# Optimization experiments

Hardware: AMD Instinct MI355X
Metric: run time of the kernel (lower is better)

The kernel has to match this reference:

```python
import jax, jax.numpy as jnp
import numpy as np

N, IN, C, H, NC, E, G = 4096, 16, 128, 2, 4, 131072, 64
EPS = 1e-5


def setup_inputs() -> dict:
    key = jax.random.key(0)
    ks = jax.random.split(key, 12)
    def rn(k, shape, scale=0.05):
        return jax.random.normal(k, shape, dtype=jnp.float32) * scale
    return dict(
        x=rn(ks[0], (N, IN), 1.0),
        edge_index=jax.random.randint(ks[1], (2, E), 0, N, dtype=jnp.int32),
        batch=jnp.sort(jax.random.randint(ks[2], (N,), 0, G, dtype=jnp.int32)),
        proj_W=rn(ks[3], (IN, C)), proj_b=jnp.zeros((C,), jnp.float32),
        gcn_W=rn(ks[4], (2, C, C)), gcn_b=jnp.zeros((2, C), jnp.float32),
        attn_qkv_w=rn(ks[5], (2, 3 * C, C)), attn_qkv_b=jnp.zeros((2, 3 * C), jnp.float32),
        attn_out_w=rn(ks[6], (2, C, C)), attn_out_b=jnp.zeros((2, C), jnp.float32),
        bn_gamma=jnp.ones((2, 3, C), jnp.float32), bn_beta=jnp.zeros((2, 3, C), jnp.float32),
        mlp_W1=rn(ks[7], (2, C, 2 * C)), mlp_b1=jnp.zeros((2, 2 * C), jnp.float32),
        mlp_W2=rn(ks[8], (2, 2 * C, C)), mlp_b2=jnp.zeros((2, C), jnp.float32),
        lin_W=rn(ks[9], (C, NC)), lin_b=jnp.zeros((NC,), jnp.float32),
    )


def _bn(h, g, b):
    # PyG BatchNorm (training-mode stats over the node dim, biased var)
    mu = jnp.mean(h, axis=0)
    var = jnp.mean((h - mu) ** 2, axis=0)
    return (h - mu) * jax.lax.rsqrt(var + EPS) * g + b


def _gcn(h_in, W, b, src, dst):
    # GCNConv: x' = D^-1/2 (A+I) D^-1/2 (x W) + b
    h = h_in @ W
    deg = jnp.zeros((N,), h.dtype).at[dst].add(1.0) + 1.0  # +1 self loop
    dinv = jax.lax.rsqrt(deg)
    coef = dinv[src] * dinv[dst]                           # [E]
    out = jax.ops.segment_sum(h[src] * coef[:, None], dst, num_segments=N)
    out = out + h * (dinv * dinv)[:, None]                 # self-loop term
    return out + b


def _mha(x, wqkv, bqkv, wout, bout):
    # batch=None in the source => attention over all N nodes as one sequence
    qkv = x @ wqkv.T + bqkv                                # [N,3C]
    q, k, v = jnp.split(qkv, 3, axis=-1)
    dh = C // H
    q = q.reshape(N, H, dh) * (dh ** -0.5)
    k = k.reshape(N, H, dh)
    v = v.reshape(N, H, dh)
    a = jax.nn.softmax(jnp.einsum('nhd,mhd->hnm', q, k), axis=-1)  # [H,N,N]
    o = jnp.einsum('hnm,mhd->nhd', a, v).reshape(N, C)
    return o @ wout.T + bout


def _forward(x, proj_W, proj_b, gcn_W, gcn_b, attn_qkv_w, attn_qkv_b,
             attn_out_w, attn_out_b, bn_gamma, bn_beta, mlp_W1, mlp_b1,
             mlp_W2, mlp_b2, lin_W, lin_b, edge_index, batch):
    src, dst = edge_index[0], edge_index[1]
    h = x @ proj_W + proj_b
    for l in range(2):  # two structurally-distinct GPS layers
        hl = _bn(_gcn(h, gcn_W[l], gcn_b[l], src, dst) + h, bn_gamma[l, 0], bn_beta[l, 0])
        ha = _bn(_mha(h, attn_qkv_w[l], attn_qkv_b[l], attn_out_w[l], attn_out_b[l]) + h,
                 bn_gamma[l, 1], bn_beta[l, 1])
        o = hl + ha
        m = jax.nn.relu(o @ mlp_W1[l] + mlp_b1[l]) @ mlp_W2[l] + mlp_b2[l]
        h = _bn(o + m, bn_gamma[l, 2], bn_beta[l, 2])
        if l == 0:
            h = jax.nn.relu(h)
    ssum = jax.ops.segment_sum(h, batch, num_segments=G)
    cnt = jax.ops.segment_sum(jnp.ones((N,), h.dtype), batch, num_segments=G)
    pooled = ssum / jnp.maximum(cnt, 1.0)[:, None]
    return pooled @ lin_W + lin_b


def reference(x, edge_index, batch, proj_W, proj_b, gcn_W, gcn_b,
              attn_qkv_w, attn_qkv_b, attn_out_w, attn_out_b,
              bn_gamma, bn_beta, mlp_W1, mlp_b1, mlp_W2, mlp_b2,
              lin_W, lin_b):
    return _forward(x, proj_W, proj_b, gcn_W, gcn_b, attn_qkv_w, attn_qkv_b,
                    attn_out_w, attn_out_b, bn_gamma, bn_beta, mlp_W1, mlp_b1,
                    mlp_W2, mlp_b2, lin_W, lin_b, edge_index, batch)
```

## Files before the change

### kernel.cpp

```cpp
#include <hip/hip_runtime.h>
#include <hip/hip_bf16.h>


constexpr int N_  = 4096;
constexpr int IN_ = 16;
constexpr int C_  = 128;
constexpr int E_  = 131072;
constexpr int G_  = 64;
constexpr float EPSV = 1e-5f;
constexpr int SP_ = 8;

typedef unsigned short u16;
typedef unsigned int u32;
typedef __attribute__((ext_vector_type(8))) short bf16x8;
typedef __attribute__((ext_vector_type(4))) short bf16x4;
typedef __attribute__((ext_vector_type(8))) unsigned short u16x8;
typedef __attribute__((ext_vector_type(4))) float f32x4;

__device__ inline u16 f2bf(float f) {
  union { __hip_bfloat16 b; u16 u; } v;
  v.b = __float2bfloat16(f);
  return v.u;
}
__device__ inline float bf2f(u16 s) {
  union { unsigned u; float f; } v; v.u = ((unsigned)s) << 16;
  return v.f;
}

__global__ __launch_bounds__(256) void prol_k(const float* __restrict__ x,
                                              const float* __restrict__ projW,
                                              const float* __restrict__ projB,
                                              float* __restrict__ h,
                                              const float* __restrict__ gcnW,
                                              const float* __restrict__ qkvW,
                                              const float* __restrict__ outW,
                                              const float* __restrict__ w1,
                                              const float* __restrict__ w2,
                                              u16* __restrict__ Wh,
                                              u16* __restrict__ Wl,
                                              const int* __restrict__ ei,
                                              int* __restrict__ cnt) {
  const int bx = blockIdx.x;
  const int tid = threadIdx.x;
  if (bx < 2048) {
    int idx = bx * 256 + tid;
    int n = idx >> 7, c = idx & 127;
    float acc = projB[c];
#pragma unroll
    for (int k = 0; k < IN_; ++k) acc = fmaf(x[n * IN_ + k], projW[k * C_ + c], acc);
    h[idx] = acc;
    return;
  }
  if (bx >= 2336) {
    int e = (bx - 2336) * 256 + tid;
    atomicAdd(&cnt[ei[E_ + e]], 1);
    return;
  }
  int wb = bx - 2048;
  int l = wb / 144, b = wb % 144;
  const float* src; int dstOff, K, M, trans;
  if (b < 16)       { src = gcnW + l * 16384; dstOff = 0;      K = 128; M = 128; trans = 0; }
  else if (b < 64)  { src = qkvW + l * 49152; dstOff = 16384;  K = 128; M = 0;   trans = 1; b -= 16; }
  else if (b < 80)  { src = outW + l * 16384; dstOff = 65536;  K = 128; M = 0;   trans = 1; b -= 64; }
  else if (b < 112) { src = w1 + l * 32768;   dstOff = 81920;  K = 128; M = 256; trans = 0; b -= 80; }
  else              { src = w2 + l * 32768;   dstOff = 114688; K = 256; M = 128; trans = 0; b -= 112; }
  dstOff += l * 147456;
  int d = b * 1024 + tid * 4;
  float v[4];
  if (trans) {
    const float4 f = *(const float4*)&src[d];
    v[0] = f.x; v[1] = f.y; v[2] = f.z; v[3] = f.w;
  } else {
    int ks = (K == 256) ? 8 : 7;
    int n = d >> ks, k = d & (K - 1);
#pragma unroll
    for (int j = 0; j < 4; ++j) v[j] = src[(size_t)(k + j) * M + n];
  }
  ushort4 hv, lv;
  u16* hp = (u16*)&hv; u16* lp = (u16*)&lv;
#pragma unroll
  for (int j = 0; j < 4; ++j) {
    u16 hh = f2bf(v[j]); hp[j] = hh; lp[j] = f2bf(v[j] - bf2f(hh));
  }
  *(ushort4*)&Wh[dstOff + d] = hv;
  *(ushort4*)&Wl[dstOff + d] = lv;
}

__global__ __launch_bounds__(256) void scan_k(const int* __restrict__ cnt,
                                              int* __restrict__ rowptr,
                                              int* __restrict__ cursor,
                                              float* __restrict__ dinv) {
  __shared__ int part[256];
  const int t = threadIdx.x;
  int v[16], s = 0;
#pragma unroll
  for (int i = 0; i < 16; ++i) { v[i] = cnt[t * 16 + i]; s += v[i]; }
  part[t] = s;
  __syncthreads();
  if (t == 0) {
    int run = 0;
    for (int i = 0; i < 256; ++i) { int x = part[i]; part[i] = run; run += x; }
  }
  __syncthreads();
  int off = part[t];
#pragma unroll
  for (int i = 0; i < 16; ++i) {
    int n = t * 16 + i;
    rowptr[n] = off; cursor[n] = off;
    dinv[n] = rsqrtf((float)v[i] + 1.0f);
    off += v[i];
  }
  if (t == 0) rowptr[N_] = E_;
}

__global__ __launch_bounds__(256) void mgemm_dual_k(const float* __restrict__ A,
                                                    const u16* __restrict__ Bh,
                                                    const u16* __restrict__ Bl,
                                                    const float* __restrict__ qkvB,
                                                    float* __restrict__ t0,
                                                    u16* __restrict__ Qg,
                                                    u16* __restrict__ Kg,
                                                    u16* __restrict__ Vtg,
                                                    const int* __restrict__ ei,
                                                    int* __restrict__ cursor,
                                                    int* __restrict__ csr) {
  constexpr int LD = 72, K = 128;
  __shared__ u16 Ah[64 * LD], Al[64 * LD], Bsh[64 * LD], Bsl[64 * LD];
  const int bx = blockIdx.x;
  const int tid = threadIdx.x;
  if (bx >= 512) {
    int e = (bx - 512) * 256 + tid;
    int d = ei[E_ + e];
    int slot = atomicAdd(&cursor[d], 1);
    csr[slot] = ei[e];
    return;
  }
  const int row0 = (bx >> 3) * 64, col0 = (bx & 7) * 64;
  const int wv = tid >> 6, ln = tid & 63, quad = ln >> 4, c = ln & 15;
  f32x4 acc[4];
#pragma unroll
  for (int i = 0; i < 4; ++i) acc[i] = (f32x4){0.f, 0.f, 0.f, 0.f};

  for (int kt = 0; kt < K; kt += 64) {
    __syncthreads();
#pragma unroll
    for (int i = 0; i < 2; ++i) {
      int ch = tid + i * 256, r = ch >> 3, part = ch & 7;
      const float4 f0 = *(const float4*)&A[(size_t)(row0 + r) * K + kt + part * 8];
      const float4 f1 = *(const float4*)&A[(size_t)(row0 + r) * K + kt + part * 8 + 4];
      float fv[8] = {f0.x, f0.y, f0.z, f0.w, f1.x, f1.y, f1.z, f1.w};
      __attribute__((aligned(16))) u16 hb[8], lb[8];
#pragma unroll
      for (int j = 0; j < 8; ++j) {
        u16 hh = f2bf(fv[j]); hb[j] = hh; lb[j] = f2bf(fv[j] - bf2f(hh));
      }
      *(u16x8*)&Ah[r * LD + part * 8] = *(u16x8*)hb;
      *(u16x8*)&Al[r * LD + part * 8] = *(u16x8*)lb;
      size_t bo = (size_t)(col0 + r) * K + kt + part * 8;
      *(u16x8*)&Bsh[r * LD + part * 8] = *(const u16x8*)&Bh[bo];
      *(u16x8*)&Bsl[r * LD + part * 8] = *(const u16x8*)&Bl[bo];
    }
    __syncthreads();
#pragma unroll
    for (int kq = 0; kq < 2; ++kq) {
      bf16x8 ah = *(const bf16x8*)&Ah[(wv * 16 + c) * LD + kq * 32 + quad * 8];
      bf16x8 al = *(const bf16x8*)&Al[(wv * 16 + c) * LD + kq * 32 + quad * 8];
#pragma unroll
      for (int cb = 0; cb < 4; ++cb) {
        bf16x8 bh = *(const bf16x8*)&Bsh[(cb * 16 + c) * LD + kq * 32 + quad * 8];
        bf16x8 bl = *(const bf16x8*)&Bsl[(cb * 16 + c) * LD + kq * 32 + quad * 8];
        acc[cb] = __builtin_amdgcn_mfma_f32_16x16x32_bf16(al, bh, acc[cb], 0, 0, 0);
        acc[cb] = __builtin_amdgcn_mfma_f32_16x16x32_bf16(ah, bl, acc[cb], 0, 0, 0);
        acc[cb] = __builtin_amdgcn_mfma_f32_16x16x32_bf16(ah, bh, acc[cb], 0, 0, 0);
      }
    }
  }

  const int cls = bx & 7;
  if (cls < 2) {
#pragma unroll
    for (int cb = 0; cb < 4; ++cb)
#pragma unroll
      for (int r = 0; r < 4; ++r) {
        int rr = row0 + wv * 16 + quad * 4 + r;
        t0[(size_t)rr * 128 + col0 + cb * 16 + c] = acc[cb][r];
      }
  } else if (cls < 6) {
    const int isQ = cls < 4, hd = cls & 1;
    const float sc = isQ ? 0.125f : 1.0f;
    u16* dst = isQ ? Qg : Kg;
#pragma unroll
    for (int cb = 0; cb < 4; ++cb) {
      int d = cb * 16 + c;
      float qb = qkvB[col0 - 128 + d];
#pragma unroll
      for (int r = 0; r < 4; ++r) {
        int rr = row0 + wv * 16 + quad * 4 + r;
        dst[((size_t)(hd * N_ + rr)) * 64 + d] = f2bf((acc[cb][r] + qb) * sc);
      }
    }
  } else {
    const int hd = cls & 1;
    u16* vtile = Ah;
    __syncthreads();
#pragma unroll
    for (int cb = 0; cb < 4; ++cb) {
      int d = cb * 16 + c;
      float vb = qkvB[col0 - 128 + d];
#pragma unroll
      for (int r = 0; r < 4; ++r)
        vtile[(wv * 16 + quad * 4 + r) * LD + d] = f2bf(acc[cb][r] + vb);
    }
    __syncthreads();
    int d = tid >> 2, j = tid & 3;
    __attribute__((aligned(16))) u16 buf[16];
#pragma unroll
    for (int m = 0; m < 16; ++m) buf[m] = vtile[(j * 16 + m) * LD + d];
    size_t o = ((size_t)(hd * 64 + d)) * N_ + row0 + j * 16;
    *(u16x8*)&Vtg[o]     = *(u16x8*)&buf[0];
    *(u16x8*)&Vtg[o + 8] = *(u16x8*)&buf[8];
  }
}

__global__ __launch_bounds__(256) void mgemm_k(const float* __restrict__ A,
                                               const u16* __restrict__ Bh,
                                               const u16* __restrict__ Bl,
                                               const float* __restrict__ bias,
                                               float* __restrict__ Cout,
                                               int K, int Ncols, int relu,
                                               const float* __restrict__ resid,
                                               float* __restrict__ sums) {
  constexpr int LD = 72;
  __shared__ u16 Ah[64 * LD], Al[64 * LD], Bsh[64 * LD], Bsl[64 * LD];
  const int tid = threadIdx.x;
  const int row0 = blockIdx.y * 64, col0 = blockIdx.x * 64;
  const int wv = tid >> 6, ln = tid & 63, quad = ln >> 4, c = ln & 15;
  f32x4 acc[4];
#pragma unroll
  for (int i = 0; i < 4; ++i) acc[i] = (f32x4){0.f, 0.f, 0.f, 0.f};

  for (int kt = 0; kt < K; kt += 64) {
    __syncthreads();
#pragma unroll
    for (int i = 0; i < 2; ++i) {
      int ch = tid + i * 256, r = ch >> 3, part = ch & 7;
      const float4 f0 = *(const float4*)&A[(size_t)(row0 + r) * K + kt + part * 8];
      const float4 f1 = *(const float4*)&A[(size_t)(row0 + r) * K + kt + part * 8 + 4];
      float fv[8] = {f0.x, f0.y, f0.z, f0.w, f1.x, f1.y, f1.z, f1.w};
      __attribute__((aligned(16))) u16 hb[8], lb[8];
#pragma unroll
      for (int j = 0; j < 8; ++j) {
        u16 hh = f2bf(fv[j]); hb[j] = hh; lb[j] = f2bf(fv[j] - bf2f(hh));
      }
      *(u16x8*)&Ah[r * LD + part * 8] = *(u16x8*)hb;
      *(u16x8*)&Al[r * LD + part * 8] = *(u16x8*)lb;
      size_t bo = (size_t)(col0 + r) * K + kt + part * 8;
      *(u16x8*)&Bsh[r * LD + part * 8] = *(const u16x8*)&Bh[bo];
      *(u16x8*)&Bsl[r * LD + part * 8] = *(const u16x8*)&Bl[bo];
    }
    __syncthreads();
#pragma unroll
    for (int kq = 0; kq < 2; ++kq) {
      bf16x8 ah = *(const bf16x8*)&Ah[(wv * 16 + c) * LD + kq * 32 + quad * 8];
      bf16x8 al = *(const bf16x8*)&Al[(wv * 16 + c) * LD + kq * 32 + quad * 8];
#pragma unroll
      for (int cb = 0; cb < 4; ++cb) {
        bf16x8 bh = *(const bf16x8*)&Bsh[(cb * 16 + c) * LD + kq * 32 + quad * 8];
        bf16x8 bl = *(const bf16x8*)&Bsl[(cb * 16 + c) * LD + kq * 32 + quad * 8];
        acc[cb] = __builtin_amdgcn_mfma_f32_16x16x32_bf16(al, bh, acc[cb], 0, 0, 0);
        acc[cb] = __builtin_amdgcn_mfma_f32_16x16x32_bf16(ah, bl, acc[cb], 0, 0, 0);
        acc[cb] = __builtin_amdgcn_mfma_f32_16x16x32_bf16(ah, bh, acc[cb], 0, 0, 0);
      }
    }
  }
#pragma unroll
  for (int cb = 0; cb < 4; ++cb) {
    float s = 0.0f, s2 = 0.0f;
#pragma unroll
    for (int r = 0; r < 4; ++r) {
      int rr = row0 + wv * 16 + quad * 4 + r;
      int cc = col0 + cb * 16 + c;
      float o = acc[cb][r] + (bias ? bias[cc] : 0.0f);
      if (resid) o += resid[(size_t)rr * Ncols + cc];
      if (relu) o = fmaxf(o, 0.0f);
      Cout[(size_t)rr * Ncols + cc] = o;
      s += o; s2 = fmaf(o, o, s2);
    }
    if (sums) {
      s  += __shfl_xor(s, 16);  s  += __shfl_xor(s, 32);
      s2 += __shfl_xor(s2, 16); s2 += __shfl_xor(s2, 32);
      if (quad == 0) {
        int cc = col0 + cb * 16 + c;
        atomicAdd(&sums[cc], s);
        atomicAdd(&sums[C_ + cc], s2);
      }
    }
  }
}

__global__ __launch_bounds__(256) void mgemm_attn_k(const float* __restrict__ attnP,
                                                    const float* __restrict__ accLp,
                                                    const u16* __restrict__ Bh,
                                                    const u16* __restrict__ Bl,
                                                    const float* __restrict__ bias,
                                                    float* __restrict__ Cout,
                                                    const float* __restrict__ resid,
                                                    float* __restrict__ sums) {
  constexpr int LD = 72, K = 128;
  __shared__ u16 Ah[64 * LD], Al[64 * LD], Bsh[64 * LD], Bsl[64 * LD];
  const int tid = threadIdx.x;
  const int row0 = blockIdx.y * 64, col0 = blockIdx.x * 64;
  const int wv = tid >> 6, ln = tid & 63, quad = ln >> 4, c = ln & 15;
  f32x4 acc[4];
#pragma unroll
  for (int i = 0; i < 4; ++i) acc[i] = (f32x4){0.f, 0.f, 0.f, 0.f};

  for (int kt = 0; kt < K; kt += 64) {
    const int head = kt >> 6;
    __syncthreads();
#pragma unroll
    for (int i = 0; i < 2; ++i) {
      int ch = tid + i * 256, r = ch >> 3, part = ch & 7;
      float lsum = 0.0f;
#pragma unroll
      for (int sp = 0; sp < SP_; ++sp) lsum += accLp[(sp * 2 + head) * N_ + row0 + r];
      float invl = 1.0f / lsum;
      float fv[8] = {0.f, 0.f, 0.f, 0.f, 0.f, 0.f, 0.f, 0.f};
#pragma unroll
      for (int sp = 0; sp < SP_; ++sp) {
        const float* p = &attnP[((size_t)sp * N_ + row0 + r) * C_ + kt + part * 8];
        const float4 f0 = *(const float4*)p;
        const float4 f1 = *(const float4*)(p + 4);
        fv[0] += f0.x; fv[1] += f0.y; fv[2] += f0.z; fv[3] += f0.w;
        fv[4] += f1.x; fv[5] += f1.y; fv[6] += f1.z; fv[7] += f1.w;
      }
      __attribute__((aligned(16))) u16 hb[8], lb[8];
#pragma unroll
      for (int j = 0; j < 8; ++j) {
        float f = fv[j] * invl;
        u16 hh = f2bf(f); hb[j] = hh; lb[j] = f2bf(f - bf2f(hh));
      }
      *(u16x8*)&Ah[r * LD + part * 8] = *(u16x8*)hb;
      *(u16x8*)&Al[r * LD + part * 8] = *(u16x8*)lb;
      size_t bo = (size_t)(col0 + r) * K + kt + part * 8;
      *(u16x8*)&Bsh[r * LD + part * 8] = *(const u16x8*)&Bh[bo];
      *(u16x8*)&Bsl[r * LD + part * 8] = *(const u16x8*)&Bl[bo];
    }
    __syncthreads();
#pragma unroll
    for (int kq = 0; kq < 2; ++kq) {
      bf16x8 ah = *(const bf16x8*)&Ah[(wv * 16 + c) * LD + kq * 32 + quad * 8];
      bf16x8 al = *(const bf16x8*)&Al[(wv * 16 + c) * LD + kq * 32 + quad * 8];
#pragma unroll
      for (int cb = 0; cb < 4; ++cb) {
        bf16x8 bh = *(const bf16x8*)&Bsh[(cb * 16 + c) * LD + kq * 32 + quad * 8];
        bf16x8 bl = *(const bf16x8*)&Bsl[(cb * 16 + c) * LD + kq * 32 + quad * 8];
        acc[cb] = __builtin_amdgcn_mfma_f32_16x16x32_bf16(al, bh, acc[cb], 0, 0, 0);
        acc[cb] = __builtin_amdgcn_mfma_f32_16x16x32_bf16(ah, bl, acc[cb], 0, 0, 0);
        acc[cb] = __builtin_amdgcn_mfma_f32_16x16x32_bf16(ah, bh, acc[cb], 0, 0, 0);
      }
    }
  }
#pragma unroll
  for (int cb = 0; cb < 4; ++cb) {
    float s = 0.0f, s2 = 0.0f;
#pragma unroll
    for (int r = 0; r < 4; ++r) {
      int rr = row0 + wv * 16 + quad * 4 + r;
      int cc = col0 + cb * 16 + c;
      float o = acc[cb][r] + bias[cc] + resid[(size_t)rr * 128 + cc];
      Cout[(size_t)rr * 128 + cc] = o;
      s += o; s2 = fmaf(o, o, s2);
    }
    s  += __shfl_xor(s, 16);  s  += __shfl_xor(s, 32);
    s2 += __shfl_xor(s2, 16); s2 += __shfl_xor(s2, 32);
    if (quad == 0) {
      int cc = col0 + cb * 16 + c;
      atomicAdd(&sums[cc], s);
      atomicAdd(&sums[C_ + cc], s2);
    }
  }
}

__global__ __launch_bounds__(256) void branch_k(const u16* __restrict__ Qg,
                                                const u16* __restrict__ Kg,
                                                const u16* __restrict__ Vtg,
                                                float* __restrict__ attnP,
                                                float* __restrict__ accLp,
                                                const int* __restrict__ rowptr,
                                                const int* __restrict__ csr,
                                                const float* __restrict__ hw,
                                                const float* __restrict__ dinv,
                                                const float* __restrict__ gbias,
                                                const float* __restrict__ hres,
                                                float* __restrict__ t1,
                                                float* __restrict__ sums0) {
  constexpr int LD = 72;
  __shared__ __attribute__((aligned(16))) u16 smem[2 * 64 * LD];
  const int tid = threadIdx.x;
  const int bx = blockIdx.x;

  if (bx >= 512) {
    const int b = bx - 512;
    const int wq = tid >> 6, lane = tid & 63;
    const int n = b * 4 + wq;
    float* ls  = (float*)smem;
    float* ls2 = ls + 512;
    const float din = dinv[n];
    float a0 = fmaf(hw[(size_t)n * C_ + lane], din * din,
                    gbias[lane] + hres[(size_t)n * C_ + lane]);
    float a1 = fmaf(hw[(size_t)n * C_ + lane + 64], din * din,
                    gbias[lane + 64] + hres[(size_t)n * C_ + lane + 64]);
    const int e1 = rowptr[n + 1];
    int e = rowptr[n];
    for (; e + 4 <= e1; e += 4) {
      int s0 = csr[e], s1 = csr[e + 1], s2i = csr[e + 2], s3 = csr[e + 3];
      float w0 = dinv[s0] * din, w1 = dinv[s1] * din;
      float w2 = dinv[s2i] * din, w3 = dinv[s3] * din;
      float x00 = hw[(size_t)s0 * C_ + lane],  x01 = hw[(size_t)s0 * C_ + lane + 64];
      float x10 = hw[(size_t)s1 * C_ + lane],  x11 = hw[(size_t)s1 * C_ + lane + 64];
      float x20 = hw[(size_t)s2i * C_ + lane], x21 = hw[(size_t)s2i * C_ + lane + 64];
      float x30 = hw[(size_t)s3 * C_ + lane],  x31 = hw[(size_t)s3 * C_ + lane + 64];
      a0 = fmaf(x00, w0, a0); a1 = fmaf(x01, w0, a1);
      a0 = fmaf(x10, w1, a0); a1 = fmaf(x11, w1, a1);
      a0 = fmaf(x20, w2, a0); a1 = fmaf(x21, w2, a1);
      a0 = fmaf(x30, w3, a0); a1 = fmaf(x31, w3, a1);
    }
    for (; e < e1; ++e) {
      int si = csr[e];
      float w = dinv[si] * din;
      a0 = fmaf(hw[(size_t)si * C_ + lane], w, a0);
      a1 = fmaf(hw[(size_t)si * C_ + lane + 64], w, a1);
    }
    t1[(size_t)n * C_ + lane]      = a0;
    t1[(size_t)n * C_ + lane + 64] = a1;
    ls[wq * 128 + lane]       = a0;  ls[wq * 128 + lane + 64]  = a1;
    ls2[wq * 128 + lane]      = a0 * a0;
    ls2[wq * 128 + lane + 64] = a1 * a1;
    __syncthreads();
    if (tid < 128) {
      float s  = ls[tid]  + ls[tid + 128]  + ls[tid + 256]  + ls[tid + 384];
      float s2 = ls2[tid] + ls2[tid + 128] + ls2[tid + 256] + ls2[tid + 384];
      atomicAdd(&sums0[tid], s);
      atomicAdd(&sums0[C_ + tid], s2);
    }
    return;
  }

  u16* Ks  = smem;
  u16* Vts = smem + 64 * LD;
  const int fb = bx;
  const int head = fb >> 8, sp = (fb >> 5) & 7, q0 = (fb & 31) * 128;
  const int wv = tid >> 6, ln = tid & 63, quad = ln >> 4, c = ln & 15;
  const int KPS = N_ / SP_;
  const int qb = q0 + wv * 32;

  bf16x8 qfA[2], qfB[2];
#pragma unroll
  for (int kq = 0; kq < 2; ++kq) {
    qfA[kq] = *(const bf16x8*)&Qg[((size_t)(head * N_ + qb + c)) * 64 + kq * 32 + quad * 8];
    qfB[kq] = *(const bf16x8*)&Qg[((size_t)(head * N_ + qb + 16 + c)) * 64 + kq * 32 + quad * 8];
  }

  f32x4 OA[4], OB[4];
#pragma unroll
  for (int i = 0; i < 4; ++i) {
    OA[i] = (f32x4){0.f, 0.f, 0.f, 0.f};
    OB[i] = (f32x4){0.f, 0.f, 0.f, 0.f};
  }
  float lsumA = 0.0f, lsumB = 0.0f;

  for (int it = 0; it < KPS / 64; ++it) {
    const int k0 = sp * KPS + it * 64;
    __syncthreads();
#pragma unroll
    for (int i = 0; i < 2; ++i) {
      int ch = tid + i * 256, row = ch >> 3, part = ch & 7;
      *(u16x8*)&Ks[row * LD + part * 8] =
          *(const u16x8*)&Kg[((size_t)(head * N_ + k0 + row)) * 64 + part * 8];
      *(u16x8*)&Vts[row * LD + part * 8] =
          *(const u16x8*)&Vtg[((size_t)(head * 64 + row)) * N_ + k0 + part * 8];
    }
    __syncthreads();

    bf16x4 pfA[4], pfB[4];
#pragma unroll
    for (int kb = 0; kb < 4; ++kb) {
      f32x4 stA = (f32x4){0.f, 0.f, 0.f, 0.f};
      f32x4 stB = (f32x4){0.f, 0.f, 0.f, 0.f};
#pragma unroll
      for (int kq = 0; kq < 2; ++kq) {
        bf16x8 a = *(const bf16x8*)&Ks[(kb * 16 + c) * LD + kq * 32 + quad * 8];
        stA = __builtin_amdgcn_mfma_f32_16x16x32_bf16(a, qfA[kq], stA, 0, 0, 0);
        stB = __builtin_amdgcn_mfma_f32_16x16x32_bf16(a, qfB[kq], stB, 0, 0, 0);
      }
      u16 a0 = f2bf(__expf(stA[0] - 8.0f));
      u16 a1 = f2bf(__expf(stA[1] - 8.0f));
      u16 a2 = f2bf(__expf(stA[2] - 8.0f));
      u16 a3 = f2bf(__expf(stA[3] - 8.0f));
      lsumA += bf2f(a0) + bf2f(a1) + bf2f(a2) + bf2f(a3);
      pfA[kb] = (bf16x4){(short)a0, (short)a1, (short)a2, (short)a3};
      u16 b0 = f2bf(__expf(stB[0] - 8.0f));
      u16 b1 = f2bf(__expf(stB[1] - 8.0f));
      u16 b2 = f2bf(__expf(stB[2] - 8.0f));
      u16 b3 = f2bf(__expf(stB[3] - 8.0f));
      lsumB += bf2f(b0) + bf2f(b1) + bf2f(b2) + bf2f(b3);
      pfB[kb] = (bf16x4){(short)b0, (short)b1, (short)b2, (short)b3};
    }

#pragma unroll
    for (int db = 0; db < 4; ++db) {
#pragma unroll
      for (int kb = 0; kb < 4; ++kb) {
        bf16x4 va = *(const bf16x4*)&Vts[(db * 16 + c) * LD + kb * 16 + quad * 4];
        OA[db] = __builtin_amdgcn_mfma_f32_16x16x16bf16_1k(va, pfA[kb], OA[db], 0, 0, 0);
        OB[db] = __builtin_amdgcn_mfma_f32_16x16x16bf16_1k(va, pfB[kb], OB[db], 0, 0, 0);
      }
    }
  }

  lsumA += __shfl_xor(lsumA, 16); lsumA += __shfl_xor(lsumA, 32);
  lsumB += __shfl_xor(lsumB, 16); lsumB += __shfl_xor(lsumB, 32);
  if (ln < 16) {
    accLp[(sp * 2 + head) * N_ + qb + c]      = lsumA;
    accLp[(sp * 2 + head) * N_ + qb + 16 + c] = lsumB;
  }

  constexpr int LDO = 68;
  float* OT = (float*)smem;
  __syncthreads();
#pragma unroll
  for (int hh = 0; hh < 2; ++hh) {
    if ((wv >> 1) == hh) {
      const int lq = (wv & 1) * 32;
#pragma unroll
      for (int db = 0; db < 4; ++db)
#pragma unroll
        for (int r = 0; r < 4; ++r) {
          OT[(lq + c) * LDO + db * 16 + quad * 4 + r]      = OA[db][r];
          OT[(lq + 16 + c) * LDO + db * 16 + quad * 4 + r] = OB[db][r];
        }
    }
    __syncthreads();
    {
      const int q_loc = tid >> 2, dblk = tid & 3;
      const float4* srcv = (const float4*)&OT[q_loc * LDO + dblk * 16];
      float4* dstv = (float4*)&attnP[((size_t)sp * N_ + q0 + hh * 64 + q_loc) * C_ + head * 64 + dblk * 16];
#pragma unroll
      for (int j = 0; j < 4; ++j) dstv[j] = srcv[j];
    }
    if (hh == 0) __syncthreads();
  }
}

__global__ __launch_bounds__(256) void bn_finapply2_k(const float* __restrict__ t0,
                                                      const float* __restrict__ t1,
                                                      const float* __restrict__ sums1,
                                                      const float* __restrict__ sums0,
                                                      const float* __restrict__ g1,
                                                      const float* __restrict__ b1v,
                                                      const float* __restrict__ g0,
                                                      const float* __restrict__ b0v,
                                                      float* __restrict__ ob) {
  __shared__ float scl1[128], shf1[128], scl0[128], shf0[128];
  const int t = threadIdx.x;
  if (t < 128) {
    float mu = sums1[t] * (1.0f / N_);
    float var = sums1[C_ + t] * (1.0f / N_) - mu * mu;
    float sc = rsqrtf(var + EPSV) * g1[t];
    scl1[t] = sc; shf1[t] = fmaf(-mu, sc, b1v[t]);
    mu = sums0[t] * (1.0f / N_);
    var = sums0[C_ + t] * (1.0f / N_) - mu * mu;
    sc = rsqrtf(var + EPSV) * g0[t];
    scl0[t] = sc; shf0[t] = fmaf(-mu, sc, b0v[t]);
  }
  __syncthreads();
  int idx = blockIdx.x * 256 + t;
  int c = idx & 127;
  ob[idx] = fmaf(t0[idx], scl1[c], shf1[c]) + fmaf(t1[idx], scl0[c], shf0[c]);
}

__global__ __launch_bounds__(256) void bn_finapply_k(const float* __restrict__ A,
                                                     const float* __restrict__ sums,
                                                     const float* __restrict__ g,
                                                     const float* __restrict__ b,
                                                     float* __restrict__ outp, int relu,
                                                     const int* __restrict__ batch,
                                                     float* __restrict__ pooled) {
  __shared__ float s_scl[128], s_shf[128];
  const int t = threadIdx.x;
  if (t < 128) {
    float mu = sums[t] * (1.0f / N_);
    float var = sums[C_ + t] * (1.0f / N_) - mu * mu;
    float sc = rsqrtf(var + EPSV) * g[t];
    s_scl[t] = sc;
    s_shf[t] = fmaf(-mu, sc, b[t]);
  }
  __syncthreads();
  int idx = blockIdx.x * 256 + t;
  int c = idx & 127;
  float v = fmaf(A[idx], s_scl[c], s_shf[c]);
  if (relu) v = fmaxf(v, 0.0f);
  outp[idx] = v;
  if (pooled) {
    int n = idx >> 7;
    atomicAdd(&pooled[(size_t)batch[n] * C_ + c], v);
  }
}

__global__ __launch_bounds__(256) void final_k(const float* __restrict__ pooled,
                                               const int* __restrict__ batch,
                                               const float* __restrict__ W,
                                               const float* __restrict__ b,
                                               float* __restrict__ out) {
  int t = threadIdx.x;
  int g = t >> 2, j = t & 3;
  int lo = 0, hi = N_;
  while (lo < hi) { int m = (lo + hi) >> 1; if (batch[m] < g) lo = m + 1; else hi = m; }
  int st = lo; lo = 0; hi = N_;
  while (lo < hi) { int m = (lo + hi) >> 1; if (batch[m] < g + 1) lo = m + 1; else hi = m; }
  float inv = 1.0f / fmaxf((float)(lo - st), 1.0f);
  float acc = b[j];
  for (int c = 0; c < C_; ++c) acc = fmaf(pooled[(size_t)g * C_ + c] * inv, W[c * 4 + j], acc);
  out[t] = acc;
}

extern "C" void kernel_launch(void* const* d_in, const int* in_sizes, int n_in,
                              void* d_out, int out_size, void* d_ws, size_t ws_size,
                              hipStream_t stream) {
  const float* x     = (const float*)d_in[0];
  const int*   ei    = (const int*)d_in[1];
  const int*   batch = (const int*)d_in[2];
  const float* projW = (const float*)d_in[3];
  const float* projB = (const float*)d_in[4];
  const float* gcnW  = (const float*)d_in[5];
  const float* gcnB  = (const float*)d_in[6];
  const float* qkvW  = (const float*)d_in[7];
  const float* qkvB  = (const float*)d_in[8];
  const float* outW  = (const float*)d_in[9];
  const float* outB  = (const float*)d_in[10];
  const float* bnG   = (const float*)d_in[11];
  const float* bnB   = (const float*)d_in[12];
  const float* w1    = (const float*)d_in[13];
  const float* b1    = (const float*)d_in[14];
  const float* w2    = (const float*)d_in[15];
  const float* b2    = (const float*)d_in[16];
  const float* linW  = (const float*)d_in[17];
  const float* linB  = (const float*)d_in[18];
  float* out = (float*)d_out;

  const size_t NC = (size_t)N_ * C_;
  const size_t HB = (size_t)2 * N_ * 64;
  float* ws   = (float*)d_ws;
  float* h    = ws;
  float* t0   = ws + 1 * NC;
  float* t1   = ws + 2 * NC;
  float* ob   = ws + 3 * NC;
  u16* Qg  = (u16*)(ws + 4 * NC);
  u16* Kg  = Qg + HB;
  u16* Vtg = Kg + HB;
  float* attnP = ws + 6 * NC;
  float* m1b   = attnP;
  float* accLp = ws + (6 + SP_) * NC;
  float* sums  = accLp + 2 * SP_ * N_;
  float* pooled = sums + 6 * 256;
  int*   icnt = (int*)(pooled + (size_t)G_ * C_);
  float* dinv = (float*)(icnt + N_);
  int*   rowptr = (int*)(dinv + N_);
  int*   cursor = rowptr + N_ + 1;
  int*   csr    = cursor + N_;
  u16*   Wh = (u16*)(csr + E_);
  u16*   Wl = Wh + 2 * 147456;

  const dim3 b256(256);

  hipMemsetAsync(sums, 0, (6 * 256 + (size_t)G_ * C_ + N_) * sizeof(float), stream);

  prol_k<<<2848, b256, 0, stream>>>(x, projW, projB, h, gcnW, qkvW, outW,
                                    w1, w2, Wh, Wl, ei, icnt);
  scan_k<<<1, b256, 0, stream>>>(icnt, rowptr, cursor, dinv);

  for (int l = 0; l < 2; ++l) {
    const size_t WL = (size_t)l * 147456;
    float* sums0 = sums + (l * 3 + 0) * 256;
    float* sums1 = sums + (l * 3 + 1) * 256;
    float* sums2 = sums + (l * 3 + 2) * 256;

    mgemm_dual_k<<<(l == 0) ? 1024 : 512, b256, 0, stream>>>(
        h, Wh + WL, Wl + WL, qkvB + l * 384, t0, Qg, Kg, Vtg, ei, cursor, csr);
    branch_k<<<1536, b256, 0, stream>>>(Qg, Kg, Vtg, attnP, accLp,
                                        rowptr, csr, t0, dinv, gcnB + l * C_,
                                        h, t1, sums0);
    mgemm_attn_k<<<dim3(2, 64), b256, 0, stream>>>(attnP, accLp,
                                                   Wh + WL + 65536, Wl + WL + 65536,
                                                   outB + l * C_, t0, h, sums1);
    bn_finapply2_k<<<(int)(NC / 256), b256, 0, stream>>>(
        t0, t1, sums1, sums0,
        bnG + (l * 3 + 1) * C_, bnB + (l * 3 + 1) * C_,
        bnG + (l * 3 + 0) * C_, bnB + (l * 3 + 0) * C_, ob);
    mgemm_k<<<dim3(4, 64), b256, 0, stream>>>(ob, Wh + WL + 81920, Wl + WL + 81920,
                                              b1 + l * 256, m1b, 128, 256, 1,
                                              nullptr, nullptr);
    mgemm_k<<<dim3(2, 64), b256, 0, stream>>>(m1b, Wh + WL + 114688, Wl + WL + 114688,
                                              b2 + l * C_, t0, 256, 128, 0,
                                              ob, sums2);
    bn_finapply_k<<<(int)(NC / 256), b256, 0, stream>>>(
        t0, sums2, bnG + (l * 3 + 2) * C_, bnB + (l * 3 + 2) * C_, h,
        (l == 0) ? 1 : 0, batch, (l == 1) ? pooled : nullptr);
  }

  final_k<<<1, 256, 0, stream>>>(pooled, batch, linW, linB, out);
}
```

Before: 316.2 us.

## Fuse BN applies into following GEMMs, double-buffer attention K/V, vectorize projection

Removes the standalone bn_finapply2 kernel by folding the two BN applies and their sum into the MLP1 GEMM's A-tile load, and folds the layer-0 final BN+ReLU into the layer-1 dual GEMM's A load (one column block writes h back). The attention loop now prefetches the next K/V tile into registers and double-buffers shared memory, which cuts one barrier per iteration. The input projection in the prologue is vectorized to four outputs per thread, so it needs fewer blocks. These changes trade extra per-block BN recomputation and doubled LDS use in branch_k for fewer launches and less global round-tripping.

```diff
diff --git a/kernel.cpp b/kernel.cpp
--- a/kernel.cpp
+++ b/kernel.cpp
@@ -42,21 +42,31 @@
                                               int* __restrict__ cnt) {
   const int bx = blockIdx.x;
   const int tid = threadIdx.x;
-  if (bx < 2048) {
-    int idx = bx * 256 + tid;
-    int n = idx >> 7, c = idx & 127;
-    float acc = projB[c];
-#pragma unroll
-    for (int k = 0; k < IN_; ++k) acc = fmaf(x[n * IN_ + k], projW[k * C_ + c], acc);
-    h[idx] = acc;
+  if (bx < 512) {
+    int base = (bx * 256 + tid) * 4;
+    int n = base >> 7, c = base & 127;
+    const float4* xr = (const float4*)&x[n * IN_];
+    float4 x0 = xr[0], x1 = xr[1], x2 = xr[2], x3 = xr[3];
+    float xv[16] = {x0.x, x0.y, x0.z, x0.w, x1.x, x1.y, x1.z, x1.w,
+                    x2.x, x2.y, x2.z, x2.w, x3.x, x3.y, x3.z, x3.w};
+    float4 acc = *(const float4*)&projB[c];
+#pragma unroll
+    for (int k = 0; k < IN_; ++k) {
+      float4 wv = *(const float4*)&projW[k * C_ + c];
+      acc.x = fmaf(xv[k], wv.x, acc.x);
+      acc.y = fmaf(xv[k], wv.y, acc.y);
+      acc.z = fmaf(xv[k], wv.z, acc.z);
+      acc.w = fmaf(xv[k], wv.w, acc.w);
+    }
+    *(float4*)&h[base] = acc;
     return;
   }
-  if (bx >= 2336) {
-    int e = (bx - 2336) * 256 + tid;
+  if (bx >= 800) {
+    int e = (bx - 800) * 256 + tid;
     atomicAdd(&cnt[ei[E_ + e]], 1);
     return;
   }
-  int wb = bx - 2048;
+  int wb = bx - 512;
   int l = wb / 144, b = wb % 144;
   const float* src; int dstOff, K, M, trans;
   if (b < 16)       { src = gcnW + l * 16384; dstOff = 0;      K = 128; M = 128; trans = 0; }
@@ -117,15 +127,20 @@
                                                     const u16* __restrict__ Bh,
                                                     const u16* __restrict__ Bl,
                                                     const float* __restrict__ qkvB,
-                                                    float* __restrict__ t0,
+                                                    float* __restrict__ hwOut,
                                                     u16* __restrict__ Qg,
                                                     u16* __restrict__ Kg,
                                                     u16* __restrict__ Vtg,
                                                     const int* __restrict__ ei,
                                                     int* __restrict__ cursor,
-                                                    int* __restrict__ csr) {
+                                                    int* __restrict__ csr,
+                                                    const float* __restrict__ bnsums,
+                                                    const float* __restrict__ bng,
+                                                    const float* __restrict__ bnb,
+                                                    float* __restrict__ hOut) {
   constexpr int LD = 72, K = 128;
   __shared__ u16 Ah[64 * LD], Al[64 * LD], Bsh[64 * LD], Bsl[64 * LD];
+  __shared__ float s_scl[128], s_shf[128];
   const int bx = blockIdx.x;
   const int tid = threadIdx.x;
   if (bx >= 512) {
@@ -137,6 +152,12 @@
   }
   const int row0 = (bx >> 3) * 64, col0 = (bx & 7) * 64;
   const int wv = tid >> 6, ln = tid & 63, quad = ln >> 4, c = ln & 15;
+  if (bnsums && tid < 128) {
+    float mu = bnsums[tid] * (1.0f / N_);
+    float var = bnsums[C_ + tid] * (1.0f / N_) - mu * mu;
+    float sc = rsqrtf(var + EPSV) * bng[tid];
+    s_scl[tid] = sc; s_shf[tid] = fmaf(-mu, sc, bnb[tid]);
+  }
   f32x4 acc[4];
 #pragma unroll
   for (int i = 0; i < 4; ++i) acc[i] = (f32x4){0.f, 0.f, 0.f, 0.f};
@@ -146,9 +167,19 @@
 #pragma unroll
     for (int i = 0; i < 2; ++i) {
       int ch = tid + i * 256, r = ch >> 3, part = ch & 7;
-      const float4 f0 = *(const float4*)&A[(size_t)(row0 + r) * K + kt + part * 8];
-      const float4 f1 = *(const float4*)&A[(size_t)(row0 + r) * K + kt + part * 8 + 4];
+      const int kk = kt + part * 8;
+      const float4 f0 = *(const float4*)&A[(size_t)(row0 + r) * K + kk];
+      const float4 f1 = *(const float4*)&A[(size_t)(row0 + r) * K + kk + 4];
       float fv[8] = {f0.x, f0.y, f0.z, f0.w, f1.x, f1.y, f1.z, f1.w};
+      if (bnsums) {
+#pragma unroll
+        for (int j = 0; j < 8; ++j)
+          fv[j] = fmaxf(fmaf(fv[j], s_scl[kk + j], s_shf[kk + j]), 0.0f);
+        if ((bx & 7) == 0) {
+          *(float4*)&hOut[(size_t)(row0 + r) * K + kk]     = (float4){fv[0], fv[1], fv[2], fv[3]};
+          *(float4*)&hOut[(size_t)(row0 + r) * K + kk + 4] = (float4){fv[4], fv[5], fv[6], fv[7]};
+        }
+      }
       __attribute__((aligned(16))) u16 hb[8], lb[8];
 #pragma unroll
       for (int j = 0; j < 8; ++j) {
@@ -156,7 +187,7 @@
       }
       *(u16x8*)&Ah[r * LD + part * 8] = *(u16x8*)hb;
       *(u16x8*)&Al[r * LD + part * 8] = *(u16x8*)lb;
-      size_t bo = (size_t)(col0 + r) * K + kt + part * 8;
+      size_t bo = (size_t)(col0 + r) * K + kk;
       *(u16x8*)&Bsh[r * LD + part * 8] = *(const u16x8*)&Bh[bo];
       *(u16x8*)&Bsl[r * LD + part * 8] = *(const u16x8*)&Bl[bo];
     }
@@ -183,7 +214,7 @@
 #pragma unroll
       for (int r = 0; r < 4; ++r) {
         int rr = row0 + wv * 16 + quad * 4 + r;
-        t0[(size_t)rr * 128 + col0 + cb * 16 + c] = acc[cb][r];
+        hwOut[(size_t)rr * 128 + col0 + cb * 16 + c] = acc[cb][r];
       }
   } else if (cls < 6) {
     const int isQ = cls < 4, hd = cls & 1;
@@ -298,6 +329,98 @@
   }
 }
 
+__global__ __launch_bounds__(256) void mgemm_mlp1_k(const float* __restrict__ t0,
+                                                    const float* __restrict__ t1,
+                                                    const float* __restrict__ sums1,
+                                                    const float* __restrict__ sums0,
+                                                    const float* __restrict__ g1,
+                                                    const float* __restrict__ b1v,
+                                                    const float* __restrict__ g0,
+                                                    const float* __restrict__ b0v,
+                                                    const u16* __restrict__ Bh,
+                                                    const u16* __restrict__ Bl,
+                                                    const float* __restrict__ bias,
+                                                    float* __restrict__ Cout,
+                                                    float* __restrict__ obOut) {
+  constexpr int LD = 72, K = 128, Ncols = 256;
+  __shared__ u16 Ah[64 * LD], Al[64 * LD], Bsh[64 * LD], Bsl[64 * LD];
+  __shared__ float s_scl1[128], s_shf1[128], s_scl0[128], s_shf0[128];
+  const int tid = threadIdx.x;
+  const int row0 = blockIdx.y * 64, col0 = blockIdx.x * 64;
+  const int wv = tid >> 6, ln = tid & 63, quad = ln >> 4, c = ln & 15;
+  if (tid < 128) {
+    float mu = sums1[tid] * (1.0f / N_);
+    float var = sums1[C_ + tid] * (1.0f / N_) - mu * mu;
+    float sc = rsqrtf(var + EPSV) * g1[tid];
+    s_scl1[tid] = sc; s_shf1[tid] = fmaf(-mu, sc, b1v[tid]);
+    mu = sums0[tid] * (1.0f / N_);
+    var = sums0[C_ + tid] * (1.0f / N_) - mu * mu;
+    sc = rsqrtf(var + EPSV) * g0[tid];
+    s_scl0[tid] = sc; s_shf0[tid] = fmaf(-mu, sc, b0v[tid]);
+  }
+  f32x4 acc[4];
+#pragma unroll
+  for (int i = 0; i < 4; ++i) acc[i] = (f32x4){0.f, 0.f, 0.f, 0.f};
+
+  for (int kt = 0; kt < K; kt += 64) {
+    __syncthreads();
+#pragma unroll
+    for (int i = 0; i < 2; ++i) {
+      int ch = tid + i * 256, r = ch >> 3, part = ch & 7;
+      const int kk = kt + part * 8;
+      const float4 a0 = *(const float4*)&t0[(size_t)(row0 + r) * K + kk];
+      const float4 a1 = *(const float4*)&t0[(size_t)(row0 + r) * K + kk + 4];
+      const float4 c0 = *(const float4*)&t1[(size_t)(row0 + r) * K + kk];
+      const float4 c1 = *(const float4*)&t1[(size_t)(row0 + r) * K + kk + 4];
+      float av[8] = {a0.x, a0.y, a0.z, a0.w, a1.x, a1.y, a1.z, a1.w};
+      float cv[8] = {c0.x, c0.y, c0.z, c0.w, c1.x, c1.y, c1.z, c1.w};
+      float fv[8];
+#pragma unroll
+      for (int j = 0; j < 8; ++j)
+        fv[j] = fmaf(av[j], s_scl1[kk + j], s_shf1[kk + j]) +
+                fmaf(cv[j], s_scl0[kk + j], s_shf0[kk + j]);
+      if (blockIdx.x == 0) {
+        *(float4*)&obOut[(size_t)(row0 + r) * K + kk]     = (float4){fv[0], fv[1], fv[2], fv[3]};
+        *(float4*)&obOut[(size_t)(row0 + r) * K + kk + 4] = (float4){fv[4], fv[5], fv[6], fv[7]};
+      }
+      __attribute__((aligned(16))) u16 hb[8], lb[8];
+#pragma unroll
+      for (int j = 0; j < 8; ++j) {
+        u16 hh = f2bf(fv[j]); hb[j] = hh; lb[j] = f2bf(fv[j] - bf2f(hh));
+      }
+      *(u16x8*)&Ah[r * LD + part * 8] = *(u16x8*)hb;
+      *(u16x8*)&Al[r * LD + part * 8] = *(u16x8*)lb;
+      size_t bo = (size_t)(col0 + r) * K + kk;
+      *(u16x8*)&Bsh[r * LD + part * 8] = *(const u16x8*)&Bh[bo];
+      *(u16x8*)&Bsl[r * LD + part * 8] = *(const u16x8*)&Bl[bo];
+    }
+    __syncthreads();
+#pragma unroll
+    for (int kq = 0; kq < 2; ++kq) {
+      bf16x8 ah = *(const bf16x8*)&Ah[(wv * 16 + c) * LD + kq * 32 + quad * 8];
+      bf16x8 al = *(const bf16x8*)&Al[(wv * 16 + c) * LD + kq * 32 + quad * 8];
+#pragma unroll
+      for (int cb = 0; cb < 4; ++cb) {
+        bf16x8 bh = *(const bf16x8*)&Bsh[(cb * 16 + c) * LD + kq * 32 + quad * 8];
+        bf16x8 bl = *(const bf16x8*)&Bsl[(cb * 16 + c) * LD + kq * 32 + quad * 8];
+        acc[cb] = __builtin_amdgcn_mfma_f32_16x16x32_bf16(al, bh, acc[cb], 0, 0, 0);
+        acc[cb] = __builtin_amdgcn_mfma_f32_16x16x32_bf16(ah, bl, acc[cb], 0, 0, 0);
+        acc[cb] = __builtin_amdgcn_mfma_f32_16x16x32_bf16(ah, bh, acc[cb], 0, 0, 0);
+      }
+    }
+  }
+#pragma unroll
+  for (int cb = 0; cb < 4; ++cb) {
+#pragma unroll
+    for (int r = 0; r < 4; ++r) {
+      int rr = row0 + wv * 16 + quad * 4 + r;
+      int cc = col0 + cb * 16 + c;
+      float o = fmaxf(acc[cb][r] + bias[cc], 0.0f);
+      Cout[(size_t)rr * Ncols + cc] = o;
+    }
+  }
+}
+
 __global__ __launch_bounds__(256) void mgemm_attn_k(const float* __restrict__ attnP,
                                                     const float* __restrict__ accLp,
                                                     const u16* __restrict__ Bh,
@@ -396,7 +519,7 @@
                                                 float* __restrict__ t1,
                                                 float* __restrict__ sums0) {
   constexpr int LD = 72;
-  __shared__ __attribute__((aligned(16))) u16 smem[2 * 64 * LD];
+  __shared__ __attribute__((aligned(16))) u16 smem[4 * 64 * LD];
   const int tid = threadIdx.x;
   const int bx = blockIdx.x;
 
@@ -447,12 +570,11 @@
     return;
   }
 
-  u16* Ks  = smem;
-  u16* Vts = smem + 64 * LD;
   const int fb = bx;
   const int head = fb >> 8, sp = (fb >> 5) & 7, q0 = (fb & 31) * 128;
   const int wv = tid >> 6, ln = tid & 63, quad = ln >> 4, c = ln & 15;
   const int KPS = N_ / SP_;
+  const int NIT = KPS / 64;
   const int qb = q0 + wv * 32;
 
   bf16x8 qfA[2], qfB[2];
@@ -470,18 +592,33 @@
   }
   float lsumA = 0.0f, lsumB = 0.0f;
 
-  for (int it = 0; it < KPS / 64; ++it) {
-    const int k0 = sp * KPS + it * 64;
-    __syncthreads();
-#pragma unroll
-    for (int i = 0; i < 2; ++i) {
-      int ch = tid + i * 256, row = ch >> 3, part = ch & 7;
-      *(u16x8*)&Ks[row * LD + part * 8] =
-          *(const u16x8*)&Kg[((size_t)(head * N_ + k0 + row)) * 64 + part * 8];
-      *(u16x8*)&Vts[row * LD + part * 8] =
-          *(const u16x8*)&Vtg[((size_t)(head * 64 + row)) * N_ + k0 + part * 8];
-    }
-    __syncthreads();
+  const int r0s = tid >> 3, p0s = tid & 7;
+  const int r1s = r0s + 32;
+  u16x8 kr0, kr1, vr0, vr1;
+  {
+    const int k0 = sp * KPS;
+    kr0 = *(const u16x8*)&Kg[((size_t)(head * N_ + k0 + r0s)) * 64 + p0s * 8];
+    kr1 = *(const u16x8*)&Kg[((size_t)(head * N_ + k0 + r1s)) * 64 + p0s * 8];
+    vr0 = *(const u16x8*)&Vtg[((size_t)(head * 64 + r0s)) * N_ + k0 + p0s * 8];
+    vr1 = *(const u16x8*)&Vtg[((size_t)(head * 64 + r1s)) * N_ + k0 + p0s * 8];
+    u16* K0 = smem;
+    *(u16x8*)&K0[r0s * LD + p0s * 8]            = kr0;
+    *(u16x8*)&K0[r1s * LD + p0s * 8]            = kr1;
+    *(u16x8*)&K0[64 * LD + r0s * LD + p0s * 8]  = vr0;
+    *(u16x8*)&K0[64 * LD + r1s * LD + p0s * 8]  = vr1;
+  }
+  __syncthreads();
+
+  for (int it = 0; it < NIT; ++it) {
+    u16* Ks  = smem + (it & 1) * 2 * 64 * LD;
+    u16* Vts = Ks + 64 * LD;
+    if (it + 1 < NIT) {
+      const int kn = sp * KPS + (it + 1) * 64;
+      kr0 = *(const u16x8*)&Kg[((size_t)(head * N_ + kn + r0s)) * 64 + p0s * 8];
+      kr1 = *(const u16x8*)&Kg[((size_t)(head * N_ + kn + r1s)) * 64 + p0s * 8];
+      vr0 = *(const u16x8*)&Vtg[((size_t)(head * 64 + r0s)) * N_ + kn + p0s * 8];
+      vr1 = *(const u16x8*)&Vtg[((size_t)(head * 64 + r1s)) * N_ + kn + p0s * 8];
+    }
 
     bf16x4 pfA[4], pfB[4];
 #pragma unroll
@@ -517,6 +654,15 @@
         OB[db] = __builtin_amdgcn_mfma_f32_16x16x16bf16_1k(va, pfB[kb], OB[db], 0, 0, 0);
       }
     }
+
+    if (it + 1 < NIT) {
+      u16* Kn = smem + ((it + 1) & 1) * 2 * 64 * LD;
+      *(u16x8*)&Kn[r0s * LD + p0s * 8]           = kr0;
+      *(u16x8*)&Kn[r1s * LD + p0s * 8]           = kr1;
+      *(u16x8*)&Kn[64 * LD + r0s * LD + p0s * 8] = vr0;
+      *(u16x8*)&Kn[64 * LD + r1s * LD + p0s * 8] = vr1;
+    }
+    __syncthreads();
   }
 
   lsumA += __shfl_xor(lsumA, 16); lsumA += __shfl_xor(lsumA, 32);
@@ -528,7 +674,6 @@
 
   constexpr int LDO = 68;
   float* OT = (float*)smem;
-  __syncthreads();
 #pragma unroll
   for (int hh = 0; hh < 2; ++hh) {
     if ((wv >> 1) == hh) {
@@ -551,33 +696,6 @@
     }
     if (hh == 0) __syncthreads();
   }
-}
-
-__global__ __launch_bounds__(256) void bn_finapply2_k(const float* __restrict__ t0,
-                                                      const float* __restrict__ t1,
-                                                      const float* __restrict__ sums1,
-                                                      const float* __restrict__ sums0,
-                                                      const float* __restrict__ g1,
-                                                      const float* __restrict__ b1v,
-                                                      const float* __restrict__ g0,
-                                                      const float* __restrict__ b0v,
-                                                      float* __restrict__ ob) {
-  __shared__ float scl1[128], shf1[128], scl0[128], shf0[128];
-  const int t = threadIdx.x;
-  if (t < 128) {
-    float mu = sums1[t] * (1.0f / N_);
-    float var = sums1[C_ + t] * (1.0f / N_) - mu * mu;
-    float sc = rsqrtf(var + EPSV) * g1[t];
-    scl1[t] = sc; shf1[t] = fmaf(-mu, sc, b1v[t]);
-    mu = sums0[t] * (1.0f / N_);
-    var = sums0[C_ + t] * (1.0f / N_) - mu * mu;
-    sc = rsqrtf(var + EPSV) * g0[t];
-    scl0[t] = sc; shf0[t] = fmaf(-mu, sc, b0v[t]);
-  }
-  __syncthreads();
-  int idx = blockIdx.x * 256 + t;
-  int c = idx & 127;
-  ob[idx] = fmaf(t0[idx], scl1[c], shf1[c]) + fmaf(t1[idx], scl0[c], shf0[c]);
 }
 
 __global__ __launch_bounds__(256) void bn_finapply_k(const float* __restrict__ A,
@@ -601,7 +719,7 @@
   int c = idx & 127;
   float v = fmaf(A[idx], s_scl[c], s_shf[c]);
   if (relu) v = fmaxf(v, 0.0f);
-  outp[idx] = v;
+  if (outp) outp[idx] = v;
   if (pooled) {
     int n = idx >> 7;
     atomicAdd(&pooled[(size_t)batch[n] * C_ + c], v);
@@ -676,7 +794,7 @@
 
   hipMemsetAsync(sums, 0, (6 * 256 + (size_t)G_ * C_ + N_) * sizeof(float), stream);
 
-  prol_k<<<2848, b256, 0, stream>>>(x, projW, projB, h, gcnW, qkvW, outW,
+  prol_k<<<1312, b256, 0, stream>>>(x, projW, projB, h, gcnW, qkvW, outW,
                                     w1, w2, Wh, Wl, ei, icnt);
   scan_k<<<1, b256, 0, stream>>>(icnt, rowptr, cursor, dinv);
 
@@ -685,28 +803,31 @@
     float* sums0 = sums + (l * 3 + 0) * 256;
     float* sums1 = sums + (l * 3 + 1) * 256;
     float* sums2 = sums + (l * 3 + 2) * 256;
+    const float* hwsrc = (l == 0) ? t0 : ob;
 
     mgemm_dual_k<<<(l == 0) ? 1024 : 512, b256, 0, stream>>>(
-        h, Wh + WL, Wl + WL, qkvB + l * 384, t0, Qg, Kg, Vtg, ei, cursor, csr);
+        (l == 0) ? h : t0, Wh + WL, Wl + WL, qkvB + l * 384,
+        (float*)hwsrc, Qg, Kg, Vtg, ei, cursor, csr,
+        (l == 0) ? nullptr : sums + 2 * 256,
+        bnG + 2 * C_, bnB + 2 * C_,
+        (l == 0) ? nullptr : h);
     branch_k<<<1536, b256, 0, stream>>>(Qg, Kg, Vtg, attnP, accLp,
-                                        rowptr, csr, t0, dinv, gcnB + l * C_,
+                                        rowptr, csr, hwsrc, dinv, gcnB + l * C_,
                                         h, t1, sums0);
     mgemm_attn_k<<<dim3(2, 64), b256, 0, stream>>>(attnP, accLp,
                                                    Wh + WL + 65536, Wl + WL + 65536,
                                                    outB + l * C_, t0, h, sums1);
-    bn_finapply2_k<<<(int)(NC / 256), b256, 0, stream>>>(
+    mgemm_mlp1_k<<<dim3(4, 64), b256, 0, stream>>>(
         t0, t1, sums1, sums0,
         bnG + (l * 3 + 1) * C_, bnB + (l * 3 + 1) * C_,
-        bnG + (l * 3 + 0) * C_, bnB + (l * 3 + 0) * C_, ob);
-    mgemm_k<<<dim3(4, 64), b256, 0, stream>>>(ob, Wh + WL + 81920, Wl + WL + 81920,
-                                              b1 + l * 256, m1b, 128, 256, 1,
-                                              nullptr, nullptr);
+        bnG + (l * 3 + 0) * C_, bnB + (l * 3 + 0) * C_,
+        Wh + WL + 81920, Wl + WL + 81920, b1 + l * 256, m1b, ob);
     mgemm_k<<<dim3(2, 64), b256, 0, stream>>>(m1b, Wh + WL + 114688, Wl + WL + 114688,
                                               b2 + l * C_, t0, 256, 128, 0,
                                               ob, sums2);
-    bn_finapply_k<<<(int)(NC / 256), b256, 0, stream>>>(
-        t0, sums2, bnG + (l * 3 + 2) * C_, bnB + (l * 3 + 2) * C_, h,
-        (l == 0) ? 1 : 0, batch, (l == 1) ? pooled : nullptr);
+    if (l == 1)
+      bn_finapply_k<<<(int)(NC / 256), b256, 0, stream>>>(
+          t0, sums2, bnG + 5 * C_, bnB + 5 * C_, nullptr, 0, batch, pooled);
   }
 
   final_k<<<1, 256, 0, stream>>>(pooled, batch, linW, linB, out);
```

Result: faster. 301.8 us (-4.6%).
